# Performance work log

Measured on AMD Instinct MI355X. Metric: run time of the kernel, lower is better.

## Reference

```python
import jax, jax.numpy as jnp
import numpy as np

MAX_LEN = 1024

def _make_pe():
    # matches TemporalPositionalEncoding buffer construction
    pe = np.zeros(MAX_LEN, np.float32)
    pos = np.arange(MAX_LEN, dtype=np.float64)
    d = MAX_LEN + 1e-9
    pe[0::2] = np.sin(pos[0::2] / 10000.0 ** (pos[0::2] / d))
    pe[1::2] = np.cos(pos[1::2] / 10000.0 ** (pos[1::2] / d))
    return jnp.asarray(pe, jnp.float32)


def setup_inputs() -> dict:
    key = jax.random.key(0)
    k1, k2, k3, k4, k5 = jax.random.split(key, 5)
    B, H, W, C = 16, 56, 56, 768
    sw = 4
    x = jax.random.normal(k1, (B, H, W, C), dtype=jnp.float32)
    # source inits these to zero; use small random weights so the op is non-trivial
    qkv_w = jax.random.normal(k2, (3 * sw, sw), dtype=jnp.float32) * 0.1
    qkv_b = jax.random.normal(k3, (3 * sw,), dtype=jnp.float32) * 0.1
    proj_w = jax.random.normal(k4, (C, C), dtype=jnp.float32) * 0.02
    proj_b = jax.random.normal(k5, (C,), dtype=jnp.float32) * 0.02
    pe = _make_pe()
    return {"x": x, "qkv_w": qkv_w, "qkv_b": qkv_b,
            "proj_w": proj_w, "proj_b": proj_b, "pe": pe}


def reference(x, qkv_w, qkv_b, proj_w, proj_b, pe):
    B, H, W, C = x.shape
    sw = qkv_w.shape[0] // 3  # group_size
    # temporal positional encoding along channel dim
    x = x + pe[:C].astype(x.dtype).reshape(1, 1, 1, -1)
    pad = (-C) % sw  # static Python int
    if pad:
        x = jnp.pad(x, ((0, 0), (0, 0), (0, 0), (0, pad)))
    Cp = x.shape[-1]
    N = Cp // sw
    xg = x.reshape(B * H * W, N, sw)  # [G, N, sw]
    qkv = xg @ qkv_w.T + qkv_b        # [G, N, 3*sw]
    q, k, v = jnp.split(qkv, 3, axis=-1)
    # SDPA with q,k,v of shape [G, N, 1, sw]: seq length (L=S=1) attention.
    # softmax over the single key is identically 1, so out == v; we keep the
    # explicit score/softmax for structural fidelity (it's scalar-per-group).
    scale = 1.0 / jnp.sqrt(jnp.asarray(sw, x.dtype))
    scores = jnp.einsum('gnd,gnd->gn', q, k) * scale          # [G, N]
    attn = jax.nn.softmax(scores[..., None, None], axis=-1)   # [G, N, 1, 1] == 1
    out = attn[..., 0] * v                                    # [G, N, sw]
    out = out.reshape(B, H, W, Cp)[..., :C]
    return out @ proj_w.T + proj_b
```

## Files before the change

kernel.cpp:

```cpp
#include <hip/hip_runtime.h>
#include <hip/hip_bf16.h>

typedef __attribute__((ext_vector_type(8))) short bf16x8;
typedef __attribute__((ext_vector_type(4))) float f32x4;
typedef __attribute__((ext_vector_type(4))) unsigned short u16x4;
typedef unsigned short u16;

#define M_DIM 50176
#define N_DIM 768
#define K_DIM 768

__device__ __forceinline__ u16 f2bf(float f) {
    __hip_bfloat16 h = __float2bfloat16(f);
    return *reinterpret_cast<u16*>(&h);
}

__device__ __forceinline__ void gld_lds16(const void* g, void* l) {
    __builtin_amdgcn_global_load_lds(
        (const __attribute__((address_space(1))) unsigned int*)g,
        (__attribute__((address_space(3))) unsigned int*)l, 16, 0, 0);
}

__global__ void fold_weights(const float* __restrict__ qkv_w,
                             const float* __restrict__ qkv_b,
                             const float* __restrict__ proj_w,
                             const float* __restrict__ proj_b,
                             const float* __restrict__ pe,
                             u16* __restrict__ Bw, float* __restrict__ bias) {
    const int o = blockIdx.x;
    const int t = threadIdx.x;
    __shared__ float wv[16];
    __shared__ float bv4[4];
    __shared__ float red[4];
    if (t < 16) wv[t] = qkv_w[32 + t];
    if (t < 4)  bv4[t] = qkv_b[8 + t];
    __syncthreads();
    const float* Prow = proj_w + o * 768;
    float s = 0.f;
    for (int c = t; c < 768; c += 256) {
        int g4 = c & ~3, j = c & 3;
        float af = Prow[g4 + 0] * wv[0 * 4 + j] + Prow[g4 + 1] * wv[1 * 4 + j] +
                   Prow[g4 + 2] * wv[2 * 4 + j] + Prow[g4 + 3] * wv[3 * 4 + j];
        Bw[o * 768 + c] = f2bf(af);
        s += af * pe[c];
        s += Prow[c] * bv4[j];
    }
    #pragma unroll
    for (int off = 32; off; off >>= 1) s += __shfl_down(s, off, 64);
    if ((t & 63) == 0) red[t >> 6] = s;
    __syncthreads();
    if (t == 0) bias[o] = red[0] + red[1] + red[2] + red[3] + proj_b[o];
}

__global__ __launch_bounds__(256, 2)
void gemm_fused(const float* __restrict__ X, const u16* __restrict__ Bw,
                const float* __restrict__ bias, float* __restrict__ Y) {
    const int b = blockIdx.x;
    const int bid = (b & 7) * 294 + (b >> 3);
    const int mt = bid / 6, nt = bid - mt * 6;
    const int m0 = mt * 128, n0 = nt * 128;

    const int tid = threadIdx.x;
    const int lane = tid & 63;
    const int w = tid >> 6;
    const int wm = w >> 1, wn = w & 1;

    __shared__ __align__(16) float pool[16384];
    u16 (*As)[128 * 64] = (u16(*)[128 * 64])pool;
    u16 (*Bs)[128 * 64] = (u16(*)[128 * 64])((char*)pool + 32768);

    f32x4 acc[4][4];
    #pragma unroll
    for (int i = 0; i < 4; ++i)
        #pragma unroll
        for (int j = 0; j < 4; ++j)
            acc[i][j] = (f32x4){0.f, 0.f, 0.f, 0.f};

    const int arow = tid >> 4;
    const int agg  = tid & 15;
    const int bg = lane & 7;

    float4 preA[8], preB[8];

    auto load_a = [&](float4 (&p)[8], int k0) {
        const float4* src = (const float4*)(X + (long)m0 * K_DIM + k0);
        #pragma unroll
        for (int i = 0; i < 8; ++i) {
            int r = arow + 16 * i;
            p[i] = src[(long)r * (K_DIM / 4) + agg];
        }
    };

    auto write_a = [&](int buf, const float4 (&p)[8]) {
        #pragma unroll
        for (int i = 0; i < 8; ++i) {
            int r = arow + 16 * i;
            int pb = (agg * 8) ^ ((r & 7) << 4);
            u16x4 hv;
            hv.x = f2bf(p[i].x);
            hv.y = f2bf(p[i].y);
            hv.z = f2bf(p[i].z);
            hv.w = f2bf(p[i].w);
            *(u16x4*)&As[buf][r * 64 + (pb >> 1)] = hv;
        }
    };

    auto stage_b = [&](int buf, int k0) {
        #pragma unroll
        for (int j = 0; j < 4; ++j) {
            int rowbase = j * 32 + w * 8;
            int row = rowbase + (lane >> 3);
            const char* src = (const char*)Bw + ((long)(n0 + row) * K_DIM + k0) * 2 +
                              ((bg * 16) ^ ((row & 7) << 4));
            gld_lds16(src, (void*)&Bs[buf][rowbase * 64]);
        }
    };

    auto compute = [&](int buf) {
        #pragma unroll
        for (int h = 0; h < 2; ++h) {
            bf16x8 av[4], bv_[4];
            #pragma unroll
            for (int mf = 0; mf < 4; ++mf) {
                int r = wm * 64 + mf * 16 + (lane & 15);
                int pb = (h * 64 + ((lane >> 4) << 4)) ^ ((r & 7) << 4);
                av[mf] = *(const bf16x8*)&As[buf][r * 64 + (pb >> 1)];
            }
            #pragma unroll
            for (int nf = 0; nf < 4; ++nf) {
                int r = wn * 64 + nf * 16 + (lane & 15);
                int pb = (h * 64 + ((lane >> 4) << 4)) ^ ((r & 7) << 4);
                bv_[nf] = *(const bf16x8*)&Bs[buf][r * 64 + (pb >> 1)];
            }
            __builtin_amdgcn_s_setprio(1);
            #pragma unroll
            for (int mf = 0; mf < 4; ++mf)
                #pragma unroll
                for (int nf = 0; nf < 4; ++nf)
                    acc[mf][nf] = __builtin_amdgcn_mfma_f32_16x16x32_bf16(
                        av[mf], bv_[nf], acc[mf][nf], 0, 0, 0);
            __builtin_amdgcn_s_setprio(0);
        }
    };

    load_a(preA, 0);
    stage_b(0, 0);
    load_a(preB, 64);
    write_a(0, preA);
    __syncthreads();

    const int NT = K_DIM / 64;
    #pragma unroll 1
    for (int t2 = 0; t2 < NT; t2 += 2) {
        if (t2 + 1 < NT) {
            write_a(1, preB);
            stage_b(1, (t2 + 1) * 64);
        }
        if (t2 + 2 < NT) load_a(preA, (t2 + 2) * 64);
        compute(0);
        __syncthreads();

        if (t2 + 2 < NT) {
            write_a(0, preA);
            stage_b(0, (t2 + 2) * 64);
        }
        if (t2 + 3 < NT) load_a(preB, (t2 + 3) * 64);
        compute(1);
        __syncthreads();
    }

    const int colq = lane & 15;
    const int rowq = (lane >> 4) * 4;
    #pragma unroll
    for (int nf = 0; nf < 4; ++nf) {
        int col = wn * 64 + nf * 16 + colq;
        float bi = bias[n0 + col];
        #pragma unroll
        for (int mf = 0; mf < 4; ++mf) {
            int rbase = wm * 64 + mf * 16 + rowq;
            #pragma unroll
            for (int r = 0; r < 4; ++r) {
                int row = rbase + r;
                int colS = col ^ (((row >> 2) & 1) << 4);
                pool[row * 128 + colS] = acc[mf][nf][r] + bi;
            }
        }
    }
    __syncthreads();

    #pragma unroll
    for (int i = 0; i < 16; ++i) {
        int chunk = i * 256 + tid;
        int row = chunk >> 5;
        int g = chunk & 31;
        int gs = g ^ (((row >> 2) & 1) << 2);
        f32x4 v = *(const f32x4*)&pool[row * 128 + gs * 4];
        __builtin_nontemporal_store(v,
            (f32x4*)&Y[(long)(m0 + row) * N_DIM + n0 + g * 4]);
    }
}

extern "C" void kernel_launch(void* const* d_in, const int* in_sizes, int n_in,
                              void* d_out, int out_size, void* d_ws, size_t ws_size,
                              hipStream_t stream) {
    const float* x      = (const float*)d_in[0];
    const float* qkv_w  = (const float*)d_in[1];
    const float* qkv_b  = (const float*)d_in[2];
    const float* proj_w = (const float*)d_in[3];
    const float* proj_b = (const float*)d_in[4];
    const float* pe     = (const float*)d_in[5];
    float* y = (float*)d_out;

    u16*   Bw   = (u16*)d_ws;
    float* bias = (float*)((char*)d_ws + (size_t)N_DIM * K_DIM * 2);

    fold_weights<<<768, 256, 0, stream>>>(qkv_w, qkv_b, proj_w, proj_b, pe, Bw, bias);
    gemm_fused<<<(M_DIM / 128) * (N_DIM / 128), 256, 0, stream>>>(x, Bw, bias, y);
}
```

Before: 100.2 us.

## Make GEMM persistent and prefetch next tile's operands during the epilogue

```diff
diff --git a/kernel.cpp b/kernel.cpp
--- a/kernel.cpp
+++ b/kernel.cpp
@@ -9,6 +9,8 @@
 #define M_DIM 50176
 #define N_DIM 768
 #define K_DIM 768
+#define NTILES 2352
+#define GRID 512
 
 __device__ __forceinline__ u16 f2bf(float f) {
     __hip_bfloat16 h = __float2bfloat16(f);
@@ -55,11 +57,6 @@
 __global__ __launch_bounds__(256, 2)
 void gemm_fused(const float* __restrict__ X, const u16* __restrict__ Bw,
                 const float* __restrict__ bias, float* __restrict__ Y) {
-    const int b = blockIdx.x;
-    const int bid = (b & 7) * 294 + (b >> 3);
-    const int mt = bid / 6, nt = bid - mt * 6;
-    const int m0 = mt * 128, n0 = nt * 128;
-
     const int tid = threadIdx.x;
     const int lane = tid & 63;
     const int w = tid >> 6;
@@ -70,11 +67,6 @@
     u16 (*Bs)[128 * 64] = (u16(*)[128 * 64])((char*)pool + 32768);
 
     f32x4 acc[4][4];
-    #pragma unroll
-    for (int i = 0; i < 4; ++i)
-        #pragma unroll
-        for (int j = 0; j < 4; ++j)
-            acc[i][j] = (f32x4){0.f, 0.f, 0.f, 0.f};
 
     const int arow = tid >> 4;
     const int agg  = tid & 15;
@@ -82,8 +74,8 @@
 
     float4 preA[8], preB[8];
 
-    auto load_a = [&](float4 (&p)[8], int k0) {
-        const float4* src = (const float4*)(X + (long)m0 * K_DIM + k0);
+    auto load_a = [&](float4 (&p)[8], const float* xbase, int k0) {
+        const float4* src = (const float4*)(xbase + k0);
         #pragma unroll
         for (int i = 0; i < 8; ++i) {
             int r = arow + 16 * i;
@@ -105,12 +97,12 @@
         }
     };
 
-    auto stage_b = [&](int buf, int k0) {
+    auto stage_b = [&](int buf, const u16* bwbase, int k0) {
         #pragma unroll
         for (int j = 0; j < 4; ++j) {
             int rowbase = j * 32 + w * 8;
             int row = rowbase + (lane >> 3);
-            const char* src = (const char*)Bw + ((long)(n0 + row) * K_DIM + k0) * 2 +
+            const char* src = (const char*)bwbase + ((long)row * K_DIM + k0) * 2 +
                               ((bg * 16) ^ ((row & 7) << 4));
             gld_lds16(src, (void*)&Bs[buf][rowbase * 64]);
         }
@@ -143,60 +135,105 @@
         }
     };
 
-    load_a(preA, 0);
-    stage_b(0, 0);
-    load_a(preB, 64);
+    auto tilecoords = [&](int t, long& m0_, int& n0_) {
+        int bid = (t & 7) * 294 + (t >> 3);
+        int mt = bid / 6, nt = bid - mt * 6;
+        m0_ = (long)mt * 128;
+        n0_ = nt * 128;
+    };
+
+    int tile = blockIdx.x;
+    long m0; int n0;
+    tilecoords(tile, m0, n0);
+    const float* xb = X + m0 * K_DIM;
+    const u16*   bb = Bw + (long)n0 * K_DIM;
+
+    load_a(preA, xb, 0);
+    stage_b(0, bb, 0);
+    load_a(preB, xb, 64);
     write_a(0, preA);
     __syncthreads();
 
-    const int NT = K_DIM / 64;
     #pragma unroll 1
-    for (int t2 = 0; t2 < NT; t2 += 2) {
-        if (t2 + 1 < NT) {
-            write_a(1, preB);
-            stage_b(1, (t2 + 1) * 64);
-        }
-        if (t2 + 2 < NT) load_a(preA, (t2 + 2) * 64);
-        compute(0);
+    for (;;) {
+        #pragma unroll
+        for (int i = 0; i < 4; ++i)
+            #pragma unroll
+            for (int j = 0; j < 4; ++j)
+                acc[i][j] = (f32x4){0.f, 0.f, 0.f, 0.f};
+
+        const int NT = K_DIM / 64;
+        #pragma unroll 1
+        for (int t2 = 0; t2 < NT; t2 += 2) {
+            if (t2 + 1 < NT) {
+                write_a(1, preB);
+                stage_b(1, bb, (t2 + 1) * 64);
+            }
+            if (t2 + 2 < NT) load_a(preA, xb, (t2 + 2) * 64);
+            compute(0);
+            __syncthreads();
+
+            if (t2 + 2 < NT) {
+                write_a(0, preA);
+                stage_b(0, bb, (t2 + 2) * 64);
+            }
+            if (t2 + 3 < NT) load_a(preB, xb, (t2 + 3) * 64);
+            compute(1);
+            __syncthreads();
+        }
+
+        int ntile = tile + GRID;
+        bool has_next = ntile < NTILES;
+        long nm0 = 0; int nn0 = 0;
+        const float* nxb = nullptr; const u16* nbb = nullptr;
+        if (has_next) {
+            tilecoords(ntile, nm0, nn0);
+            nxb = X + nm0 * K_DIM;
+            nbb = Bw + (long)nn0 * K_DIM;
+            load_a(preA, nxb, 0);
+            load_a(preB, nxb, 64);
+            stage_b(0, nbb, 0);
+        }
+
+        const int colq = lane & 15;
+        const int rowq = (lane >> 4) * 4;
+        #pragma unroll
+        for (int p = 0; p < 2; ++p) {
+            if (wm == p) {
+                #pragma unroll
+                for (int nf = 0; nf < 4; ++nf) {
+                    int col = wn * 64 + nf * 16 + colq;
+                    float bi = bias[n0 + col];
+                    #pragma unroll
+                    for (int mf = 0; mf < 4; ++mf) {
+                        #pragma unroll
+                        for (int r = 0; r < 4; ++r) {
+                            int rl = mf * 16 + rowq + r;
+                            int colS = col ^ (((rl >> 2) & 1) << 4);
+                            pool[rl * 128 + colS] = acc[mf][nf][r] + bi;
+                        }
+                    }
+                }
+            }
+            __syncthreads();
+            #pragma unroll
+            for (int i = 0; i < 8; ++i) {
+                int chunk = i * 256 + tid;
+                int rl = chunk >> 5;
+                int g = chunk & 31;
+                int gs = g ^ (((rl >> 2) & 1) << 2);
+                f32x4 v = *(const f32x4*)&pool[rl * 128 + gs * 4];
+                __builtin_nontemporal_store(v,
+                    (f32x4*)&Y[(m0 + p * 64 + rl) * N_DIM + n0 + g * 4]);
+            }
+            __syncthreads();
+        }
+
+        if (!has_next) return;
+
+        write_a(0, preA);
         __syncthreads();
-
-        if (t2 + 2 < NT) {
-            write_a(0, preA);
-            stage_b(0, (t2 + 2) * 64);
-        }
-        if (t2 + 3 < NT) load_a(preB, (t2 + 3) * 64);
-        compute(1);
-        __syncthreads();
-    }
-
-    const int colq = lane & 15;
-    const int rowq = (lane >> 4) * 4;
-    #pragma unroll
-    for (int nf = 0; nf < 4; ++nf) {
-        int col = wn * 64 + nf * 16 + colq;
-        float bi = bias[n0 + col];
-        #pragma unroll
-        for (int mf = 0; mf < 4; ++mf) {
-            int rbase = wm * 64 + mf * 16 + rowq;
-            #pragma unroll
-            for (int r = 0; r < 4; ++r) {
-                int row = rbase + r;
-                int colS = col ^ (((row >> 2) & 1) << 4);
-                pool[row * 128 + colS] = acc[mf][nf][r] + bi;
-            }
-        }
-    }
-    __syncthreads();
-
-    #pragma unroll
-    for (int i = 0; i < 16; ++i) {
-        int chunk = i * 256 + tid;
-        int row = chunk >> 5;
-        int g = chunk & 31;
-        int gs = g ^ (((row >> 2) & 1) << 2);
-        f32x4 v = *(const f32x4*)&pool[row * 128 + gs * 4];
-        __builtin_nontemporal_store(v,
-            (f32x4*)&Y[(long)(m0 + row) * N_DIM + n0 + g * 4]);
+        tile = ntile; m0 = nm0; n0 = nn0; xb = nxb; bb = nbb;
     }
 }
 
@@ -215,5 +252,5 @@
     float* bias = (float*)((char*)d_ws + (size_t)N_DIM * K_DIM * 2);
 
     fold_weights<<<768, 256, 0, stream>>>(qkv_w, qkv_b, proj_w, proj_b, pe, Bw, bias);
-    gemm_fused<<<(M_DIM / 128) * (N_DIM / 128), 256, 0, stream>>>(x, Bw, bias, y);
-}
+    gemm_fused<<<GRID, 256, 0, stream>>>(x, Bw, bias, y);
+}
```

Measured after the change: 112.9 us. 12.7% more time.
